# Performance work log

Hardware: AMD Instinct MI355X
Metric: run time of the kernel (lower is better)

Reference implementation:

```python
import jax, jax.numpy as jnp
import numpy as np

N = 100000      # nodes
F_IN = 500      # num_features
H = 128         # num_hidden
C = 40          # num_classes
E = 3200000     # structural edges
K = 5           # knn neighbors


def setup_inputs() -> dict:
    key = jax.random.key(0)
    ks = jax.random.split(key, 9)
    x = jax.random.normal(ks[0], (N, F_IN), dtype=jnp.float32)
    edge_index = jax.random.randint(ks[1], (2, E), 0, N, dtype=jnp.int64)
    # knn graph: source i repeated K times, targets random (stand-in for cosine-KNN)
    src = jnp.repeat(jnp.arange(N, dtype=jnp.int64), K)
    dst = jax.random.randint(ks[2], (K * N,), 0, N, dtype=jnp.int64)
    edge_index_knn = jnp.stack([src, dst])
    s = lambda f: np.float32(1.0 / np.sqrt(f))
    W1 = jax.random.normal(ks[3], (F_IN, H), jnp.float32) * s(F_IN)
    b1 = jnp.zeros((H,), jnp.float32)
    W2 = jax.random.normal(ks[4], (2 * H, C), jnp.float32) * s(2 * H)
    b2 = jnp.zeros((C,), jnp.float32)
    Wlin = jax.random.normal(ks[5], (C, 2 * C), jnp.float32) * s(2 * C)  # torch Linear layout [out,in]
    blin = jnp.zeros((C,), jnp.float32)
    return {"x": x, "edge_index": edge_index, "edge_index_knn": edge_index_knn,
            "W1": W1, "b1": b1, "W2": W2, "b2": b2, "Wlin": Wlin, "blin": blin}


def gcn_conv(x, W, b, edge_index):
    # PyG GCNConv: add self-loops, symmetric normalization deg^-1/2 A deg^-1/2, x@W, scatter-add, +bias
    n = x.shape[0]
    loop = jnp.arange(n, dtype=edge_index.dtype)
    row = jnp.concatenate([edge_index[0], loop])  # sources (gathered)
    col = jnp.concatenate([edge_index[1], loop])  # targets (scattered)
    deg = jax.ops.segment_sum(jnp.ones_like(col, x.dtype), col, num_segments=n)
    dinv = jnp.where(deg > 0, jax.lax.rsqrt(jnp.maximum(deg, 1e-12)), 0.0).astype(x.dtype)
    norm = dinv[row] * dinv[col]                      # [E+n]
    h = x @ W                                          # [n, out]
    agg = jax.ops.segment_sum(h[row] * norm[:, None], col, num_segments=n)
    return agg + b


def reference(x, edge_index, edge_index_knn, W1, b1, W2, b2, Wlin, blin):
    h1 = gcn_conv(x, W1, b1, edge_index)
    h1_2 = gcn_conv(x, W1, b1, edge_index_knn)
    R1 = jax.nn.relu(jnp.concatenate([h1, h1_2], axis=1))  # dropout identity (eval mode)
    h2 = gcn_conv(R1, W2, b2, edge_index)
    h2_2 = gcn_conv(R1, W2, b2, edge_index_knn)
    R2 = jnp.concatenate([h2, h2_2], axis=1)
    logits = R2 @ Wlin.T + blin
    return jax.nn.log_softmax(logits, axis=1)
```

## Files before the change

### kernel.cpp

```cpp
#include <hip/hip_runtime.h>
#include <stdint.h>

#define NN   100000
#define FIN  500
#define HID  128
#define KP1  512
#define K2   256
#define CO   40
#define NPQ  80
#define NPQP 128
#define NBUCK 391
#define CAPB_S 9216
#define CAPB_K 1536

typedef __attribute__((ext_vector_type(8))) short short8;
typedef __attribute__((ext_vector_type(4))) float float4v;
typedef __attribute__((address_space(3))) unsigned int as3_u32;
typedef __attribute__((address_space(1))) unsigned int as1_u32;

__device__ __forceinline__ unsigned short f2bf(float f) {
  unsigned u = __float_as_uint(f);
  u = u + 0x7fffu + ((u >> 16) & 1u);
  return (unsigned short)(u >> 16);
}
__device__ __forceinline__ float bf2f(unsigned short s) {
  return __uint_as_float(((unsigned)s) << 16);
}
__device__ __forceinline__ void gl_lds16(const void* g, void* l) {
  __builtin_amdgcn_global_load_lds((const as1_u32*)g, (as3_u32*)l, 16, 0, 0);
}

__global__ __launch_bounds__(256) void k_binw(
    const int* __restrict__ ei, int nS, int nb1S, int* __restrict__ gcur_s, int* __restrict__ gbin_s,
    const int* __restrict__ eik, int nK, int nbBin, int* __restrict__ gcur_k, int* __restrict__ gbin_k,
    const float* __restrict__ W1, unsigned short* __restrict__ W1T,
    const float* __restrict__ W2, const float* __restrict__ Wl,
    const float* __restrict__ b2, const float* __restrict__ bl,
    unsigned short* __restrict__ WpqT, float* __restrict__ cb) {
  __shared__ int cnt[NBUCK];
  __shared__ int base[NBUCK];
  const int t = threadIdx.x;

  if (blockIdx.x >= nbBin) {
    const int wb = blockIdx.x - nbBin;
    if (wb < 256) {
      const int idx = wb * 256 + t;
      const int n = idx >> 9, k = idx & 511;
      const float v = (k < FIN) ? W1[k * HID + n] : 0.f;
      W1T[idx] = f2bf(v);
    } else {
      const int lb = wb - 256;
      const int idx = lb * 256 + t;
      const int n = idx >> 8, k = idx & 255;
      const int o = (n < CO) ? n : n - CO;
      const int joff = (n < CO) ? 0 : CO;
      float s = 0.f;
#pragma unroll 8
      for (int j = 0; j < CO; ++j) s += W2[k * CO + j] * Wl[o * NPQ + joff + j];
      WpqT[n * K2 + k] = f2bf(s);
      if (lb == 0 && t < CO) {
        const int oo = t;
        float c = bl[oo];
        for (int j = 0; j < CO; ++j) c += b2[j] * (Wl[oo * NPQ + j] + Wl[oo * NPQ + CO + j]);
        cb[oo] = c;
      }
    }
    return;
  }

  const int b = blockIdx.x;
  const bool knn = (b >= nb1S);
  const int* src = knn ? eik      : ei;
  const int* tgt = knn ? eik + nK : ei + nS;
  const int n    = knn ? nK : nS;
  int* gcur      = knn ? gcur_k : gcur_s;
  int* gbin      = knn ? gbin_k : gbin_s;
  const int capb = knn ? CAPB_K : CAPB_S;
  const int ebase = (knn ? b - nb1S : b) * 4096;

  for (int i = t; i < NBUCK; i += 256) cnt[i] = 0;
  __syncthreads();
  int s[16], g[16];
#pragma unroll
  for (int i = 0; i < 16; ++i) {
    const int e = ebase + i * 256 + t;
    const bool v = e < n;
    s[i] = v ? src[e] : 0;
    g[i] = v ? tgt[e] : -1;
    if (v) atomicAdd(&cnt[g[i] >> 8], 1);
  }
  __syncthreads();
  for (int i = t; i < NBUCK; i += 256) {
    const int c = cnt[i];
    base[i] = c ? atomicAdd(&gcur[i], c) : 0;
    cnt[i] = 0;
  }
  __syncthreads();
#pragma unroll
  for (int i = 0; i < 16; ++i) {
    if (g[i] >= 0) {
      const int bkt = g[i] >> 8;
      const int pos = base[bkt] + atomicAdd(&cnt[bkt], 1);
      if (pos < capb) gbin[bkt * capb + pos] = (s[i] << 8) | (g[i] & 255);
    }
  }
}

__global__ __launch_bounds__(512) void k_bscan(const int* __restrict__ gcur_s, int* __restrict__ bscan_s,
                                               const int* __restrict__ gcur_k, int* __restrict__ bscan_k) {
  __shared__ int sd[512];
  const int* gcur = blockIdx.x ? gcur_k : gcur_s;
  int* bscan      = blockIdx.x ? bscan_k : bscan_s;
  const int t = threadIdx.x;
  const int v = (t < NBUCK) ? gcur[t] : 0;
  sd[t] = v;
  __syncthreads();
  for (int off = 1; off < 512; off <<= 1) {
    const int x = (t >= off) ? sd[t - off] : 0;
    __syncthreads(); sd[t] += x; __syncthreads();
  }
  if (t < NBUCK) bscan[t] = sd[t] - v;
}

union SMemCG {
  struct { int cnt[256]; int base[256]; } c;
  struct { float A[2][2048]; unsigned short B[2][4096]; } g;
};

__global__ __launch_bounds__(256) void k_csrg1(
    const int* __restrict__ gcur_s, const int* __restrict__ gbin_s, const int* __restrict__ bscan_s,
    int* __restrict__ rp_s, int2* __restrict__ colw_s, float* __restrict__ dinv_s,
    const int* __restrict__ gcur_k, const int* __restrict__ gbin_k, const int* __restrict__ bscan_k,
    int* __restrict__ rp_k, int2* __restrict__ colw_k, float* __restrict__ dinv_k,
    const float* __restrict__ x, const unsigned short* __restrict__ W1T,
    const float* __restrict__ zbuf, unsigned short* __restrict__ H1b) {
  __shared__ SMemCG sm;
  const int t = threadIdx.x;

  if (blockIdx.x < 2 * NBUCK) {
    int* cnt  = sm.c.cnt;
    int* base = sm.c.base;
    const int b0 = blockIdx.x;
    const bool knn = (b0 >= NBUCK);
    const int b = knn ? b0 - NBUCK : b0;
    const int* gcur  = knn ? gcur_k  : gcur_s;
    const int* gbin  = knn ? gbin_k  : gbin_s;
    const int* bscan = knn ? bscan_k : bscan_s;
    int* rp     = knn ? rp_k   : rp_s;
    int2* colw  = knn ? colw_k : colw_s;
    float* dinv = knn ? dinv_k : dinv_s;
    const int capb = knn ? CAPB_K : CAPB_S;
    int nB = gcur[b]; if (nB > capb) nB = capb;
    const int gb0 = b * capb;
    const int gbase = bscan[b];

    cnt[t] = 0;
    __syncthreads();
    for (int i = t; i < nB; i += 256) atomicAdd(&cnt[gbin[gb0 + i] & 255], 1);
    __syncthreads();
    const int myc = cnt[t];
    base[t] = myc;
    __syncthreads();
    for (int off = 1; off < 256; off <<= 1) {
      const int x2 = (t >= off) ? base[t - off] : 0;
      __syncthreads(); base[t] += x2; __syncthreads();
    }
    const int excl = base[t] - myc;
    const int tg = b * 256 + t;
    if (tg < NN) { rp[tg] = gbase + excl; dinv[tg] = rsqrtf((float)(myc + 1)); }
    if (tg == NN) rp[NN] = gbase + excl;
    __syncthreads();
    base[t] = excl; cnt[t] = 0;
    __syncthreads();
    for (int i = t; i < nB; i += 256) {
      const int e = gbin[gb0 + i];
      const int tl = e & 255;
      const int pos = atomicAdd(&cnt[tl], 1);
      colw[gbase + base[tl] + pos] = make_int2(e >> 8, 0);
    }
    return;
  }

  const int wv = t >> 6, lane = t & 63;
  const int qd = lane >> 4, mr = lane & 15;
  const int m0 = (blockIdx.x - 2 * NBUCK) * 64;

  float4v acc[8];
  const float4v zf4 = {0.f, 0.f, 0.f, 0.f};
#pragma unroll
  for (int b = 0; b < 8; ++b) acc[b] = zf4;

  auto stage = [&](int kk, int pb) {
    const int k0 = kk * 32;
#pragma unroll
    for (int i = 0; i < 2; ++i) {
      const int q = (wv * 2 + i) * 64 + lane;
      const int m = q >> 3;
      const int kg = (q & 7) ^ (m & 7);
      const int gm = m0 + m, kb = k0 + kg * 4;
      const float* gp = (gm < NN && kb < FIN) ? (x + (size_t)gm * FIN + kb) : zbuf;
      gl_lds16(gp, &sm.g.A[pb][q * 4]);
    }
#pragma unroll
    for (int i = 0; i < 2; ++i) {
      const int q = (wv * 2 + i) * 64 + lane;
      const int n = q >> 2;
      const int kg = (q & 3) ^ ((q >> 3) & 3);
      gl_lds16(W1T + n * KP1 + k0 + kg * 8, &sm.g.B[pb][q * 8]);
    }
  };

  stage(0, 0);
  for (int kk = 0; kk < 16; ++kk) {
    const int cur = kk & 1;
    if (kk + 1 < 16) {
      stage(kk + 1, cur ^ 1);
      asm volatile("s_waitcnt vmcnt(4)" ::: "memory");
    } else {
      asm volatile("s_waitcnt vmcnt(0)" ::: "memory");
    }
    __builtin_amdgcn_s_barrier();

    short8 af;
    {
      const int m = wv * 16 + mr;
      const int s0 = m * 8 + ((2 * qd) ^ (m & 7));
      const int s1 = m * 8 + ((2 * qd + 1) ^ (m & 7));
      const float4v a0 = *(const float4v*)&sm.g.A[cur][s0 * 4];
      const float4v a1 = *(const float4v*)&sm.g.A[cur][s1 * 4];
      af[0] = (short)f2bf(a0[0]); af[1] = (short)f2bf(a0[1]);
      af[2] = (short)f2bf(a0[2]); af[3] = (short)f2bf(a0[3]);
      af[4] = (short)f2bf(a1[0]); af[5] = (short)f2bf(a1[1]);
      af[6] = (short)f2bf(a1[2]); af[7] = (short)f2bf(a1[3]);
    }
#pragma unroll
    for (int ct = 0; ct < 8; ++ct) {
      const int n = ct * 16 + mr;
      const int sb = n * 4 + (qd ^ ((n >> 1) & 3));
      const short8 bf = *(const short8*)&sm.g.B[cur][sb * 8];
      acc[ct] = __builtin_amdgcn_mfma_f32_16x16x32_bf16(af, bf, acc[ct], 0, 0, 0);
    }
    __builtin_amdgcn_s_barrier();
  }

  const int rb = m0 + wv * 16 + qd * 4;
#pragma unroll
  for (int ct = 0; ct < 8; ++ct) {
    const int col = ct * 16 + mr;
#pragma unroll
    for (int j = 0; j < 4; ++j) {
      const int r = rb + j;
      if (r < NN) H1b[(size_t)r * HID + col] = f2bf(acc[ct][j]);
    }
  }
}

__global__ __launch_bounds__(256) void k_fuse(
    int2* __restrict__ colw_s, const float* __restrict__ dinv_s, int nS, int nbF,
    int2* __restrict__ colw_k, const float* __restrict__ dinv_k, int nK) {
  const int b = blockIdx.x;
  if (b < nbF) {
    const int i = b * 256 + threadIdx.x;
    if (i < nS) {
      const int s = colw_s[i].x;
      colw_s[i].y = __float_as_int(dinv_s[s]);
    }
  } else {
    const int i = (b - nbF) * 256 + threadIdx.x;
    if (i < nK) {
      const int s = colw_k[i].x;
      colw_k[i].y = __float_as_int(dinv_k[s]);
    }
  }
}

__global__ __launch_bounds__(256) void k_gemm2(const unsigned short* __restrict__ R1b,
    const unsigned short* __restrict__ WpqT, const unsigned short* __restrict__ zbuf,
    unsigned short* __restrict__ PQ) {
  __shared__ unsigned short Als[2][256 * 8];
  __shared__ unsigned short Bls[2][512 * 8];
  const int t = threadIdx.x;
  const int wv = t >> 6, lane = t & 63;
  const int qd = lane >> 4, mr = lane & 15;
  const int m0 = blockIdx.x * 64;

  float4v acc[5];
  const float4v zf4 = {0.f, 0.f, 0.f, 0.f};
#pragma unroll
  for (int b = 0; b < 5; ++b) acc[b] = zf4;

  auto stage = [&](int kk, int pb) {
    const int k0 = kk * 32;
    {
      const int q = wv * 64 + lane;
      const int m = q >> 2;
      const int kg = (q & 3) ^ ((q >> 3) & 3);
      const int gm = m0 + m;
      const unsigned short* gp = (gm < NN) ? (R1b + (size_t)gm * K2 + k0 + kg * 8) : zbuf;
      gl_lds16(gp, &Als[pb][q * 8]);
    }
#pragma unroll
    for (int i = 0; i < 2; ++i) {
      const int q = (wv * 2 + i) * 64 + lane;
      const int n = q >> 2;
      const int kg = (q & 3) ^ ((q >> 3) & 3);
      gl_lds16(WpqT + n * K2 + k0 + kg * 8, &Bls[pb][q * 8]);
    }
  };

  stage(0, 0);
  for (int kk = 0; kk < 8; ++kk) {
    const int cur = kk & 1;
    if (kk + 1 < 8) {
      stage(kk + 1, cur ^ 1);
      asm volatile("s_waitcnt vmcnt(3)" ::: "memory");
    } else {
      asm volatile("s_waitcnt vmcnt(0)" ::: "memory");
    }
    __builtin_amdgcn_s_barrier();

    short8 af;
    {
      const int m = wv * 16 + mr;
      const int sa = m * 4 + (qd ^ ((m >> 1) & 3));
      af = *(const short8*)&Als[cur][sa * 8];
    }
#pragma unroll
    for (int ct = 0; ct < 5; ++ct) {
      const int n = ct * 16 + mr;
      const int sb = n * 4 + (qd ^ ((n >> 1) & 3));
      const short8 bf = *(const short8*)&Bls[cur][sb * 8];
      acc[ct] = __builtin_amdgcn_mfma_f32_16x16x32_bf16(af, bf, acc[ct], 0, 0, 0);
    }
    __builtin_amdgcn_s_barrier();
  }

  const int rb = m0 + wv * 16 + qd * 4;
#pragma unroll
  for (int ct = 0; ct < 5; ++ct) {
    const int col = ct * 16 + mr;
#pragma unroll
    for (int j = 0; j < 4; ++j) {
      const int r = rb + j;
      if (r < NN) PQ[(size_t)r * NPQ + col] = f2bf(acc[ct][j]);
    }
  }
}

__device__ __forceinline__ void ld8(const int2* __restrict__ cw, int base, int e1, bool full,
                                    int2* __restrict__ q) {
  if (full) {
#pragma unroll
    for (int j = 0; j < 8; ++j) q[j] = cw[base + j];
  } else {
    const int e1c = e1 - 1;
#pragma unroll
    for (int j = 0; j < 8; ++j) {
      const int ee = base + j;
      int2 t = cw[(ee < e1) ? ee : e1c];
      t.y = (ee < e1) ? t.y : 0;
      q[j] = t;
    }
  }
}
__device__ __forceinline__ void g8(const int2* __restrict__ q,
    const unsigned* __restrict__ H32, int lane, unsigned* __restrict__ d) {
#pragma unroll
  for (int j = 0; j < 8; ++j) d[j] = H32[(size_t)q[j].x * 64 + lane];
}
__device__ __forceinline__ void f8(const int2* __restrict__ q, const unsigned* __restrict__ d,
                                   float& ax, float& ay) {
#pragma unroll
  for (int j = 0; j < 8; ++j) {
    const float w = __int_as_float(q[j].y);
    ax += w * __uint_as_float(d[j] << 16);
    ay += w * __uint_as_float(d[j] & 0xffff0000u);
  }
}

__global__ __launch_bounds__(256) void k_agg1(
    const int* __restrict__ rp_s, const int2* __restrict__ colw_s, const float* __restrict__ dinv_s,
    const int* __restrict__ rp_k, const int2* __restrict__ colw_k, const float* __restrict__ dinv_k,
    const unsigned short* __restrict__ H, const float* __restrict__ bias,
    unsigned short* __restrict__ out) {
  const int wv = threadIdx.x >> 6, lane = threadIdx.x & 63;
  const int c = blockIdx.x * 4 + wv;
  if (c >= NN) return;
  const unsigned* H32 = (const unsigned*)H;
  const int e0s = __builtin_amdgcn_readfirstlane(rp_s[c]);
  const int e1s = __builtin_amdgcn_readfirstlane(rp_s[c + 1]);
  const int e0k = __builtin_amdgcn_readfirstlane(rp_k[c]);
  const int e1k = __builtin_amdgcn_readfirstlane(rp_k[c + 1]);
  const int nbS = (e1s - e0s + 7) >> 3;
  const int nbK = (e1k - e0k + 7) >> 3;

  int2 q0[8], q1[8], qk[8];
  unsigned d0[8], d1[8], dk[8];
  const unsigned pc = H32[(size_t)c * 64 + lane];
  if (nbS > 0) { ld8(colw_s, e0s, e1s, e0s + 8 <= e1s, q0); g8(q0, H32, lane, d0); }
  if (nbS > 1) { ld8(colw_s, e0s + 8, e1s, e0s + 16 <= e1s, q1); g8(q1, H32, lane, d1); }
  if (nbK > 0) { ld8(colw_k, e0k, e1k, e0k + 8 <= e1k, qk); g8(qk, H32, lane, dk); }

  const float dcs = dinv_s[c], dck = dinv_k[c];
  const float slo = __uint_as_float(pc << 16);
  const float shi = __uint_as_float(pc & 0xffff0000u);
  float ax = dcs * slo, ay = dcs * shi;
  float bx = dck * slo, by = dck * shi;

  int b = 0;
  while (b + 2 < nbS) {
    f8(q0, d0, ax, ay);
    {
      const int bs = e0s + (b + 2) * 8;
      ld8(colw_s, bs, e1s, bs + 8 <= e1s, q0);
      g8(q0, H32, lane, d0);
    }
    f8(q1, d1, ax, ay);
    if (b + 3 < nbS) {
      const int bs = e0s + (b + 3) * 8;
      ld8(colw_s, bs, e1s, bs + 8 <= e1s, q1);
      g8(q1, H32, lane, d1);
    }
    b += 2;
  }
  if (b < nbS) f8(q0, d0, ax, ay);
  if (b + 1 < nbS) f8(q1, d1, ax, ay);

  if (nbK > 0) f8(qk, dk, bx, by);
  for (int bk = 1; bk < nbK; ++bk) {
    const int bs = e0k + bk * 8;
    ld8(colw_k, bs, e1k, bs + 8 <= e1k, qk);
    g8(qk, H32, lane, dk);
    f8(qk, dk, bx, by);
  }

  const float2 bb = ((const float2*)bias)[lane];
  const float o0 = fmaxf(dcs * ax + bb.x, 0.f);
  const float o1 = fmaxf(dcs * ay + bb.y, 0.f);
  const float o2 = fmaxf(dck * bx + bb.x, 0.f);
  const float o3 = fmaxf(dck * by + bb.y, 0.f);
  unsigned* orow = (unsigned*)(out + (size_t)c * K2);
  orow[lane]      = (unsigned)f2bf(o0) | ((unsigned)f2bf(o1) << 16);
  orow[64 + lane] = (unsigned)f2bf(o2) | ((unsigned)f2bf(o3) << 16);
}

__device__ __forceinline__ void ld12(const int2* __restrict__ cw, int base, int e1, bool full,
                                     int2* __restrict__ q) {
  if (full) {
#pragma unroll
    for (int j = 0; j < 12; ++j) q[j] = cw[base + j];
  } else {
    const int e1c = e1 - 1;
#pragma unroll
    for (int j = 0; j < 12; ++j) {
      const int ee = base + j;
      int2 t = cw[(ee < e1) ? ee : e1c];
      t.y = (ee < e1) ? t.y : 0;
      q[j] = t;
    }
  }
}
__device__ __forceinline__ void gt4(const int2* __restrict__ q, const unsigned* __restrict__ PQ32,
                                    int g, int l, int off, float* __restrict__ w,
                                    unsigned* __restrict__ d) {
#pragma unroll
  for (int t = 0; t < 4; ++t) {
    const int2 qa = q[3 * t], qb = q[3 * t + 1], qc = q[3 * t + 2];
    const int xs = (g == 0) ? qa.x : ((g == 1) ? qb.x : qc.x);
    const int wi = (g == 0) ? qa.y : ((g == 1) ? qb.y : qc.y);
    w[t] = __int_as_float(wi);
    d[t] = PQ32[(size_t)xs * 40 + off + l];
  }
}
__device__ __forceinline__ void ct4(const float* __restrict__ w, const unsigned* __restrict__ d,
                                    float& sx, float& sy) {
#pragma unroll
  for (int t = 0; t < 4; ++t) {
    sx += w[t] * __uint_as_float(d[t] << 16);
    sy += w[t] * __uint_as_float(d[t] & 0xffff0000u);
  }
}

__global__ __launch_bounds__(256) void k_aggf(
    const int* __restrict__ rp_s, const int2* __restrict__ colw_s, const float* __restrict__ dinv_s,
    const int* __restrict__ rp_k, const int2* __restrict__ colw_k, const float* __restrict__ dinv_k,
    const unsigned short* __restrict__ PQ, const float* __restrict__ cb,
    float* __restrict__ out) {
  const int wv = threadIdx.x >> 6, lane = threadIdx.x & 63;
  const int c = blockIdx.x * 4 + wv;
  if (c >= NN) return;
  const unsigned* PQ32 = (const unsigned*)PQ;
  const int g = (lane < 60) ? (lane / 20) : 2;
  const int l = lane - 20 * g;

  const int e0s = __builtin_amdgcn_readfirstlane(rp_s[c]);
  const int e1s = __builtin_amdgcn_readfirstlane(rp_s[c + 1]);
  const int e0k = __builtin_amdgcn_readfirstlane(rp_k[c]);
  const int e1k = __builtin_amdgcn_readfirstlane(rp_k[c + 1]);
  const int nbS = (e1s - e0s + 11) / 12;
  const int nbK = (e1k - e0k + 11) / 12;

  unsigned dP = 0, dQ = 0;
  if (lane < 20) {
    dP = PQ32[(size_t)c * 40 + lane];
    dQ = PQ32[(size_t)c * 40 + 20 + lane];
  }

  int2 q0[12], q1[12], qk[12];
  float w0[4], w1[4], wk[4];
  unsigned d0[4], d1[4], dk[4];
  if (nbS > 0) { ld12(colw_s, e0s, e1s, e0s + 12 <= e1s, q0); gt4(q0, PQ32, g, l, 0, w0, d0); }
  if (nbS > 1) { ld12(colw_s, e0s + 12, e1s, e0s + 24 <= e1s, q1); gt4(q1, PQ32, g, l, 0, w1, d1); }
  if (nbK > 0) { ld12(colw_k, e0k, e1k, e0k + 12 <= e1k, qk); gt4(qk, PQ32, g, l, 20, wk, dk); }

  float sx = 0.f, sy = 0.f, kx = 0.f, ky = 0.f;
  int b = 0;
  while (b + 2 < nbS) {
    ct4(w0, d0, sx, sy);
    {
      const int bs = e0s + (b + 2) * 12;
      ld12(colw_s, bs, e1s, bs + 12 <= e1s, q0);
      gt4(q0, PQ32, g, l, 0, w0, d0);
    }
    ct4(w1, d1, sx, sy);
    if (b + 3 < nbS) {
      const int bs = e0s + (b + 3) * 12;
      ld12(colw_s, bs, e1s, bs + 12 <= e1s, q1);
      gt4(q1, PQ32, g, l, 0, w1, d1);
    }
    b += 2;
  }
  if (b < nbS) ct4(w0, d0, sx, sy);
  if (b + 1 < nbS) ct4(w1, d1, sx, sy);

  if (nbK > 0) ct4(wk, dk, kx, ky);
  for (int bk = 1; bk < nbK; ++bk) {
    const int bs = e0k + bk * 12;
    ld12(colw_k, bs, e1k, bs + 12 <= e1k, qk);
    gt4(qk, PQ32, g, l, 20, wk, dk);
    ct4(wk, dk, kx, ky);
  }

  sx += __shfl(sx, lane + 20) + __shfl(sx, lane + 40);
  sy += __shfl(sy, lane + 20) + __shfl(sy, lane + 40);
  kx += __shfl(kx, lane + 20) + __shfl(kx, lane + 40);
  ky += __shfl(ky, lane + 20) + __shfl(ky, lane + 40);

  float lo = 0.f, hi = 0.f;
  if (lane < 20) {
    const float dcs = dinv_s[c], dck = dinv_k[c];
    const float2 cbb = ((const float2*)cb)[lane];
    lo = dcs * (sx + dcs * __uint_as_float(dP << 16))
       + dck * (kx + dck * __uint_as_float(dQ << 16)) + cbb.x;
    hi = dcs * (sy + dcs * __uint_as_float(dP & 0xffff0000u))
       + dck * (ky + dck * __uint_as_float(dQ & 0xffff0000u)) + cbb.y;
  }
  float m = (lane < 20) ? fmaxf(lo, hi) : -3.4e38f;
#pragma unroll
  for (int off = 1; off < 64; off <<= 1) m = fmaxf(m, __shfl_xor(m, off));
  float s = (lane < 20) ? (expf(lo - m) + expf(hi - m)) : 0.f;
#pragma unroll
  for (int off = 1; off < 64; off <<= 1) s += __shfl_xor(s, off);
  const float lse = m + logf(s);
  if (lane < 20) {
    float2 o; o.x = lo - lse; o.y = hi - lse;
    ((float2*)(out + (size_t)c * CO))[lane] = o;
  }
}

extern "C" void kernel_launch(void* const* d_in, const int* in_sizes, int n_in,
                              void* d_out, int out_size, void* d_ws, size_t ws_size,
                              hipStream_t stream) {
  const float* x  = (const float*)d_in[0];
  const int* ei   = (const int*)d_in[1];
  const int* eik  = (const int*)d_in[2];
  const float* W1 = (const float*)d_in[3];
  const float* b1 = (const float*)d_in[4];
  const float* W2 = (const float*)d_in[5];
  const float* b2 = (const float*)d_in[6];
  const float* Wl = (const float*)d_in[7];
  const float* bl = (const float*)d_in[8];
  float* out = (float*)d_out;
  const int E  = in_sizes[1] / 2;
  const int EK = in_sizes[2] / 2;

  char* p = (char*)d_ws;
  size_t off = 0;
  auto alloc = [&](size_t bytes) -> void* {
    void* r = (void*)(p + off);
    off += (bytes + 255) & ~(size_t)255;
    return r;
  };
  int* gcur_s = (int*)alloc((size_t)NBUCK * 4);
  int* gcur_k = (int*)alloc((size_t)NBUCK * 4);
  void* zbuf = alloc(256);
  const size_t zero_span = off;
  int* bscan_s = (int*)alloc((size_t)NBUCK * 4);
  int* bscan_k = (int*)alloc((size_t)NBUCK * 4);
  float* dinv_s = (float*)alloc((size_t)NN * 4);
  float* dinv_k = (float*)alloc((size_t)NN * 4);
  int* rp_s = (int*)alloc((size_t)(NN + 1) * 4);
  int* rp_k = (int*)alloc((size_t)(NN + 1) * 4);
  unsigned short* W1T = (unsigned short*)alloc((size_t)HID * KP1 * 2);
  unsigned short* WpqT = (unsigned short*)alloc((size_t)NPQP * K2 * 2);
  float* cbv = (float*)alloc((size_t)CO * 4);
  int* gbin_s = (int*)alloc((size_t)NBUCK * CAPB_S * 4);
  int* gbin_k = (int*)alloc((size_t)NBUCK * CAPB_K * 4);
  int2* colw_s = (int2*)alloc((size_t)E * 8);
  int2* colw_k = (int2*)alloc((size_t)EK * 8);
  unsigned short* H1b = (unsigned short*)alloc((size_t)NN * HID * 2);
  unsigned short* R1b = (unsigned short*)alloc((size_t)NN * K2 * 2);
  unsigned short* PQ = H1b;

  hipMemsetAsync(d_ws, 0, zero_span, stream);

  const int nb1S = (E + 4095) / 4096;
  const int nb1K = (EK + 4095) / 4096;
  const int nbBin = nb1S + nb1K;
  k_binw<<<nbBin + 256 + NPQ, 256, 0, stream>>>(
      ei, E, nb1S, gcur_s, gbin_s, eik, EK, nbBin, gcur_k, gbin_k,
      W1, W1T, W2, Wl, b2, bl, WpqT, cbv);
  k_bscan<<<2, 512, 0, stream>>>(gcur_s, bscan_s, gcur_k, bscan_k);

  const int nbG1 = (NN + 63) / 64;
  k_csrg1<<<2 * NBUCK + nbG1, 256, 0, stream>>>(
      gcur_s, gbin_s, bscan_s, rp_s, colw_s, dinv_s,
      gcur_k, gbin_k, bscan_k, rp_k, colw_k, dinv_k,
      x, W1T, (const float*)zbuf, H1b);

  const int nbF = (E + 255) / 256;
  const int nbFk = (EK + 255) / 256;
  k_fuse<<<nbF + nbFk, 256, 0, stream>>>(colw_s, dinv_s, E, nbF, colw_k, dinv_k, EK);

  const int nbAgg = (NN + 3) / 4;
  k_agg1<<<nbAgg, 256, 0, stream>>>(rp_s, colw_s, dinv_s, rp_k, colw_k, dinv_k, H1b, b1, R1b);

  k_gemm2<<<(NN + 63) / 64, 256, 0, stream>>>(R1b, WpqT, (const unsigned short*)zbuf, PQ);
  k_aggf<<<nbAgg, 256, 0, stream>>>(rp_s, colw_s, dinv_s, rp_k, colw_k, dinv_k, PQ, cbv, out);
}
```

Measured before the change: 669.7 us.

## Compute degrees during binning and fuse dinv into CSR build, dropping k_fuse

Per-node in-degrees are now counted with global atomics during the binning pass, and dinv is computed in the scan kernel from those counts. The CSR build then reads the degree directly instead of recounting from bins, and writes the source's dinv alongside each column index, so the separate k_fuse pass over all edges goes away. The cost is 3.3M extra global atomics in k_binw, a gathered dinv read during CSR construction, and 800 KB more workspace to zero with memset.

```diff
diff --git a/kernel.cpp b/kernel.cpp
--- a/kernel.cpp
+++ b/kernel.cpp
@@ -33,6 +33,7 @@
 __global__ __launch_bounds__(256) void k_binw(
     const int* __restrict__ ei, int nS, int nb1S, int* __restrict__ gcur_s, int* __restrict__ gbin_s,
     const int* __restrict__ eik, int nK, int nbBin, int* __restrict__ gcur_k, int* __restrict__ gbin_k,
+    int* __restrict__ deg_s, int* __restrict__ deg_k,
     const float* __restrict__ W1, unsigned short* __restrict__ W1T,
     const float* __restrict__ W2, const float* __restrict__ Wl,
     const float* __restrict__ b2, const float* __restrict__ bl,
@@ -75,6 +76,7 @@
   const int n    = knn ? nK : nS;
   int* gcur      = knn ? gcur_k : gcur_s;
   int* gbin      = knn ? gbin_k : gbin_s;
+  int* deg       = knn ? deg_k  : deg_s;
   const int capb = knn ? CAPB_K : CAPB_S;
   const int ebase = (knn ? b - nb1S : b) * 4096;
 
@@ -87,7 +89,10 @@
     const bool v = e < n;
     s[i] = v ? src[e] : 0;
     g[i] = v ? tgt[e] : -1;
-    if (v) atomicAdd(&cnt[g[i] >> 8], 1);
+    if (v) {
+      atomicAdd(&cnt[g[i] >> 8], 1);
+      atomicAdd(&deg[g[i]], 1);
+    }
   }
   __syncthreads();
   for (int i = t; i < NBUCK; i += 256) {
@@ -106,12 +111,21 @@
   }
 }
 
-__global__ __launch_bounds__(512) void k_bscan(const int* __restrict__ gcur_s, int* __restrict__ bscan_s,
-                                               const int* __restrict__ gcur_k, int* __restrict__ bscan_k) {
+__global__ __launch_bounds__(512) void k_scand(
+    const int* __restrict__ gcur_s, int* __restrict__ bscan_s,
+    const int* __restrict__ gcur_k, int* __restrict__ bscan_k,
+    const int* __restrict__ deg_s, float* __restrict__ dinv_s,
+    const int* __restrict__ deg_k, float* __restrict__ dinv_k) {
   __shared__ int sd[512];
+  const int t = threadIdx.x;
+  if (blockIdx.x >= 2) {
+    const int i = (blockIdx.x - 2) * 512 + t;
+    if (i < NN) dinv_s[i] = rsqrtf((float)(deg_s[i] + 1));
+    else if (i < 2 * NN) dinv_k[i - NN] = rsqrtf((float)(deg_k[i - NN] + 1));
+    return;
+  }
   const int* gcur = blockIdx.x ? gcur_k : gcur_s;
   int* bscan      = blockIdx.x ? bscan_k : bscan_s;
-  const int t = threadIdx.x;
   const int v = (t < NBUCK) ? gcur[t] : 0;
   sd[t] = v;
   __syncthreads();
@@ -129,9 +143,11 @@
 
 __global__ __launch_bounds__(256) void k_csrg1(
     const int* __restrict__ gcur_s, const int* __restrict__ gbin_s, const int* __restrict__ bscan_s,
-    int* __restrict__ rp_s, int2* __restrict__ colw_s, float* __restrict__ dinv_s,
+    int* __restrict__ rp_s, int2* __restrict__ colw_s,
+    const int* __restrict__ deg_s, const float* __restrict__ dinv_s,
     const int* __restrict__ gcur_k, const int* __restrict__ gbin_k, const int* __restrict__ bscan_k,
-    int* __restrict__ rp_k, int2* __restrict__ colw_k, float* __restrict__ dinv_k,
+    int* __restrict__ rp_k, int2* __restrict__ colw_k,
+    const int* __restrict__ deg_k, const float* __restrict__ dinv_k,
     const float* __restrict__ x, const unsigned short* __restrict__ W1T,
     const float* __restrict__ zbuf, unsigned short* __restrict__ H1b) {
   __shared__ SMemCG sm;
@@ -146,19 +162,17 @@
     const int* gcur  = knn ? gcur_k  : gcur_s;
     const int* gbin  = knn ? gbin_k  : gbin_s;
     const int* bscan = knn ? bscan_k : bscan_s;
+    const int* deg   = knn ? deg_k   : deg_s;
+    const float* dv  = knn ? dinv_k  : dinv_s;
     int* rp     = knn ? rp_k   : rp_s;
     int2* colw  = knn ? colw_k : colw_s;
-    float* dinv = knn ? dinv_k : dinv_s;
     const int capb = knn ? CAPB_K : CAPB_S;
     int nB = gcur[b]; if (nB > capb) nB = capb;
     const int gb0 = b * capb;
     const int gbase = bscan[b];
-
-    cnt[t] = 0;
-    __syncthreads();
-    for (int i = t; i < nB; i += 256) atomicAdd(&cnt[gbin[gb0 + i] & 255], 1);
-    __syncthreads();
-    const int myc = cnt[t];
+    const int tg = b * 256 + t;
+
+    const int myc = (tg < NN) ? deg[tg] : 0;
     base[t] = myc;
     __syncthreads();
     for (int off = 1; off < 256; off <<= 1) {
@@ -166,8 +180,7 @@
       __syncthreads(); base[t] += x2; __syncthreads();
     }
     const int excl = base[t] - myc;
-    const int tg = b * 256 + t;
-    if (tg < NN) { rp[tg] = gbase + excl; dinv[tg] = rsqrtf((float)(myc + 1)); }
+    if (tg < NN) rp[tg] = gbase + excl;
     if (tg == NN) rp[NN] = gbase + excl;
     __syncthreads();
     base[t] = excl; cnt[t] = 0;
@@ -175,8 +188,9 @@
     for (int i = t; i < nB; i += 256) {
       const int e = gbin[gb0 + i];
       const int tl = e & 255;
+      const int srcn = e >> 8;
       const int pos = atomicAdd(&cnt[tl], 1);
-      colw[gbase + base[tl] + pos] = make_int2(e >> 8, 0);
+      colw[gbase + base[tl] + pos] = make_int2(srcn, __float_as_int(dv[srcn]));
     }
     return;
   }
@@ -251,25 +265,6 @@
     for (int j = 0; j < 4; ++j) {
       const int r = rb + j;
       if (r < NN) H1b[(size_t)r * HID + col] = f2bf(acc[ct][j]);
-    }
-  }
-}
-
-__global__ __launch_bounds__(256) void k_fuse(
-    int2* __restrict__ colw_s, const float* __restrict__ dinv_s, int nS, int nbF,
-    int2* __restrict__ colw_k, const float* __restrict__ dinv_k, int nK) {
-  const int b = blockIdx.x;
-  if (b < nbF) {
-    const int i = b * 256 + threadIdx.x;
-    if (i < nS) {
-      const int s = colw_s[i].x;
-      colw_s[i].y = __float_as_int(dinv_s[s]);
-    }
-  } else {
-    const int i = (b - nbF) * 256 + threadIdx.x;
-    if (i < nK) {
-      const int s = colw_k[i].x;
-      colw_k[i].y = __float_as_int(dinv_k[s]);
     }
   }
 }
@@ -593,6 +588,8 @@
   };
   int* gcur_s = (int*)alloc((size_t)NBUCK * 4);
   int* gcur_k = (int*)alloc((size_t)NBUCK * 4);
+  int* deg_s  = (int*)alloc((size_t)NN * 4);
+  int* deg_k  = (int*)alloc((size_t)NN * 4);
   void* zbuf = alloc(256);
   const size_t zero_span = off;
   int* bscan_s = (int*)alloc((size_t)NBUCK * 4);
@@ -619,18 +616,17 @@
   const int nbBin = nb1S + nb1K;
   k_binw<<<nbBin + 256 + NPQ, 256, 0, stream>>>(
       ei, E, nb1S, gcur_s, gbin_s, eik, EK, nbBin, gcur_k, gbin_k,
-      W1, W1T, W2, Wl, b2, bl, WpqT, cbv);
-  k_bscan<<<2, 512, 0, stream>>>(gcur_s, bscan_s, gcur_k, bscan_k);
+      deg_s, deg_k, W1, W1T, W2, Wl, b2, bl, WpqT, cbv);
+
+  const int nbD = (2 * NN + 511) / 512;
+  k_scand<<<2 + nbD, 512, 0, stream>>>(gcur_s, bscan_s, gcur_k, bscan_k,
+                                       deg_s, dinv_s, deg_k, dinv_k);
 
   const int nbG1 = (NN + 63) / 64;
   k_csrg1<<<2 * NBUCK + nbG1, 256, 0, stream>>>(
-      gcur_s, gbin_s, bscan_s, rp_s, colw_s, dinv_s,
-      gcur_k, gbin_k, bscan_k, rp_k, colw_k, dinv_k,
+      gcur_s, gbin_s, bscan_s, rp_s, colw_s, deg_s, dinv_s,
+      gcur_k, gbin_k, bscan_k, rp_k, colw_k, deg_k, dinv_k,
       x, W1T, (const float*)zbuf, H1b);
-
-  const int nbF = (E + 255) / 256;
-  const int nbFk = (EK + 255) / 256;
-  k_fuse<<<nbF + nbFk, 256, 0, stream>>>(colw_s, dinv_s, E, nbF, colw_k, dinv_k, EK);
 
   const int nbAgg = (NN + 3) / 4;
   k_agg1<<<nbAgg, 256, 0, stream>>>(rp_s, colw_s, dinv_s, rp_k, colw_k, dinv_k, H1b, b1, R1b);
```

Result: slower. 778.1 us (+16.2%).
